# Kernel optimization log

Hardware: AMD Instinct MI355X
Metric: run time of the kernel (lower is better)

The kernel has to match this reference:

```python
import jax, jax.numpy as jnp
import numpy as np

EPS = 1e-5

def _layernorm(x, g, b):
    m = jnp.mean(x, axis=-1, keepdims=True)
    v = jnp.mean((x - m) ** 2, axis=-1, keepdims=True)
    return (x - m) * jax.lax.rsqrt(v + EPS) * g + b

def setup_inputs() -> dict:
    key = jax.random.key(0)
    ks = jax.random.split(key, 6)
    b, s, n = 1, 256, 512
    dim_msa, dim_pair, heads, dim_head = 64, 128, 8, 32
    dim_inner = heads * dim_head
    msa = jax.random.normal(ks[0], (b, s, n, dim_msa), dtype=jnp.float32)
    pairwise_repr = jax.random.normal(ks[1], (b, n, n, dim_pair), dtype=jnp.float32)
    mask = jnp.ones((b, n), dtype=bool)
    return {
        "msa": msa,
        "pairwise_repr": pairwise_repr,
        "ln_msa_g": jnp.ones((dim_msa,), jnp.float32),
        "ln_msa_b": jnp.zeros((dim_msa,), jnp.float32),
        "W_vg": jax.random.normal(ks[2], (dim_msa, dim_inner * 2), jnp.float32) * 0.02,
        "ln_pair_g": jnp.ones((dim_pair,), jnp.float32),
        "ln_pair_b": jnp.zeros((dim_pair,), jnp.float32),
        "W_pair": jax.random.normal(ks[3], (dim_pair, heads), jnp.float32) * 0.02,
        "W_out": jax.random.normal(ks[4], (dim_inner, dim_msa), jnp.float32) * 0.02,
        "mask": mask,
    }

def reference(msa, pairwise_repr, ln_msa_g, ln_msa_b, W_vg, ln_pair_g, ln_pair_b, W_pair, W_out, mask):
    heads, dim_head = 8, 32
    b, s, n, dim_msa = msa.shape
    # values and gates: LN -> LinearNoBias -> split (gv h d)
    vg = _layernorm(msa, ln_msa_g, ln_msa_b) @ W_vg            # [b,s,n,2*h*d]
    vg = vg.reshape(b, s, n, 2, heads, dim_head)
    vg = jnp.transpose(vg, (3, 0, 4, 1, 2, 5))                  # [2,b,h,s,n,d]
    values, gates = vg[0], jax.nn.sigmoid(vg[1])
    # pair bias: LN -> LinearNoBias -> [b,h,i,j]
    bias = _layernorm(pairwise_repr, ln_pair_g, ln_pair_b) @ W_pair  # [b,i,j,h]
    bias = jnp.transpose(bias, (0, 3, 1, 2))                    # [b,h,i,j]
    bias = jnp.where(mask[:, None, None, :], bias, -jnp.inf)
    weights = jax.nn.softmax(bias, axis=-1)                     # [b,h,i,j]
    out = jnp.einsum('bhij,bhsjd->bhsid', weights, values)      # [b,h,s,n,d]
    out = out * gates
    out = jnp.transpose(out, (0, 2, 3, 1, 4)).reshape(b, s, n, heads * dim_head)
    return out @ W_out                                          # [b,s,n,dim_msa]
```

## Files before the change

kernel.cpp:

```cpp
#include <hip/hip_runtime.h>
#include <hip/hip_bf16.h>


#define S 256
#define N 512
#define DM 64
#define DP 128
#define H 8
#define C 256
#define ROWS (S * N)

typedef __attribute__((ext_vector_type(8))) short bf16x8;
typedef __attribute__((ext_vector_type(4))) float f32x4;

static __device__ __forceinline__ float bf2f(unsigned int u16) {
    union { unsigned int i; float f; } x;
    x.i = u16 << 16;
    return x.f;
}
static __device__ __forceinline__ unsigned short f2bf(float f) {
    union { float f; unsigned int i; } x;
    x.f = f;
    unsigned int r = x.i + 0x7FFFu + ((x.i >> 16) & 1u);
    return (unsigned short)(r >> 16);
}
static __device__ __forceinline__ void gload16(const void* g, void* l) {
    __builtin_amdgcn_global_load_lds(
        (const __attribute__((address_space(1))) void*)g,
        (__attribute__((address_space(3))) void*)l, 16, 0, 0);
}

__global__ __launch_bounds__(256) void k0_prep(
    const float* __restrict__ Wvg, const float* __restrict__ g, const float* __restrict__ b,
    const float* __restrict__ Wout, const float* __restrict__ gp, const float* __restrict__ bp,
    const float* __restrict__ Wp,
    unsigned short* __restrict__ WTvg, float* __restrict__ biasvg, unsigned short* __restrict__ WoutT,
    float* __restrict__ Wg, float* __restrict__ sgcb)
{
    const int t = threadIdx.x;
    if (blockIdx.x < 2) {
        const int c = blockIdx.x * 256 + t;
        float bias = 0.f;
        unsigned short row[64];
#pragma unroll
        for (int k = 0; k < 64; k++) {
            const float w = Wvg[k * 512 + c];
            row[k] = f2bf(w * g[k]);
            bias = fmaf(w, b[k], bias);
        }
#pragma unroll
        for (int q = 0; q < 8; q++) *(uint4*)(WTvg + c * 64 + q * 8) = *(const uint4*)(row + q * 8);
        biasvg[c] = bias;
    } else if (blockIdx.x == 2) {
        const int m = t >> 2, c0 = (t & 3) * 64;
        unsigned short row[64];
#pragma unroll
        for (int q = 0; q < 64; q++) row[q] = f2bf(Wout[(c0 + q) * 64 + m]);
#pragma unroll
        for (int q = 0; q < 8; q++) *(uint4*)(WoutT + m * 256 + c0 + q * 8) = *(const uint4*)(row + q * 8);
    } else {
        if (t < 128) {
            const float gm = gp[t];
#pragma unroll
            for (int h = 0; h < 8; h++) Wg[t * 8 + h] = gm * Wp[t * 8 + h];
        } else if (t < 136) {
            const int h = t - 128;
            float sg = 0.f, cb = 0.f;
            for (int k = 0; k < 128; k++) {
                sg = fmaf(gp[k], Wp[k * 8 + h], sg);
                cb = fmaf(bp[k], Wp[k * 8 + h], cb);
            }
            sgcb[h] = sg;
            sgcb[8 + h] = cb;
        }
    }
}

__global__ __launch_bounds__(512, 4) void k1_vg_mfma(
    const float* __restrict__ msa, const unsigned short* __restrict__ WTvg,
    const float* __restrict__ biasvg,
    unsigned short* __restrict__ VT, unsigned short* __restrict__ G)
{
    __shared__ unsigned short wt[512 * 64];
    __shared__ unsigned short at[64 * 64];
    const int t = threadIdx.x, lane = t & 63, w = t >> 6;
    const int l15 = lane & 15, lgrp = lane >> 4;
    const int s = blockIdx.x >> 1;
    const int jbase = (blockIdx.x & 1) * 256;

#pragma unroll
    for (int q = 0; q < 8; q++) {
        const int u = q * 512 + t;
        const int c = u >> 3, ch = u & 7;
        const uint4 v = *(const uint4*)(WTvg + c * 64 + ch * 8);
        *(uint4*)((char*)wt + c * 128 + ((ch ^ (c & 7)) * 16)) = v;
    }
    float biasr[4];
    float bias2[4][4];
    if (w < 4) {
#pragma unroll
        for (int cf = 0; cf < 4; cf++) biasr[cf] = biasvg[w * 64 + cf * 16 + l15];
    } else {
#pragma unroll
        for (int cf = 0; cf < 4; cf++)
#pragma unroll
            for (int r = 0; r < 4; r++) bias2[cf][r] = biasvg[w * 64 + cf * 16 + lgrp * 4 + r];
    }

    for (int tile = 0; tile < 4; ++tile) {
        const int j0 = jbase + tile * 64;
        {
            const int r = t >> 3, kc = (t & 7) * 8;
            const float* src = msa + ((size_t)(s * 512 + j0 + r)) * 64 + kc;
            const float4 x0 = *(const float4*)src;
            const float4 x1 = *(const float4*)(src + 4);
            float s1 = x0.x + x0.y + x0.z + x0.w + x1.x + x1.y + x1.z + x1.w;
            float s2 = x0.x * x0.x + x0.y * x0.y + x0.z * x0.z + x0.w * x0.w
                     + x1.x * x1.x + x1.y * x1.y + x1.z * x1.z + x1.w * x1.w;
#pragma unroll
            for (int off = 1; off < 8; off <<= 1) {
                s1 += __shfl_xor(s1, off);
                s2 += __shfl_xor(s2, off);
            }
            const float m = s1 * (1.f / 64.f);
            const float inv = rsqrtf(s2 * (1.f / 64.f) - m * m + 1e-5f);
            unsigned short buf[8];
            buf[0] = f2bf((x0.x - m) * inv); buf[1] = f2bf((x0.y - m) * inv);
            buf[2] = f2bf((x0.z - m) * inv); buf[3] = f2bf((x0.w - m) * inv);
            buf[4] = f2bf((x1.x - m) * inv); buf[5] = f2bf((x1.y - m) * inv);
            buf[6] = f2bf((x1.z - m) * inv); buf[7] = f2bf((x1.w - m) * inv);
            *(uint4*)((char*)at + r * 128 + (((t & 7) ^ (r & 7)) * 16)) = *(const uint4*)buf;
        }
        __syncthreads();

        f32x4 acc[4][4];
#pragma unroll
        for (int rf = 0; rf < 4; rf++)
#pragma unroll
            for (int cf = 0; cf < 4; cf++) acc[rf][cf] = (f32x4){0.f, 0.f, 0.f, 0.f};

#pragma unroll
        for (int ks = 0; ks < 2; ks++) {
            bf16x8 bfr[4];
#pragma unroll
            for (int cf = 0; cf < 4; cf++) {
                const int c = w * 64 + cf * 16 + l15;
                bfr[cf] = *(const bf16x8*)((const char*)wt + c * 128 + (((ks * 4 + lgrp) ^ (c & 7)) * 16));
            }
#pragma unroll
            for (int rf = 0; rf < 4; rf++) {
                const int rr = rf * 16 + l15;
                const bf16x8 afr = *(const bf16x8*)((const char*)at + rr * 128 + (((ks * 4 + lgrp) ^ (rr & 7)) * 16));
                if (w < 4) {
#pragma unroll
                    for (int cf = 0; cf < 4; cf++)
                        acc[rf][cf] = __builtin_amdgcn_mfma_f32_16x16x32_bf16(afr, bfr[cf], acc[rf][cf], 0, 0, 0);
                } else {
#pragma unroll
                    for (int cf = 0; cf < 4; cf++)
                        acc[rf][cf] = __builtin_amdgcn_mfma_f32_16x16x32_bf16(bfr[cf], afr, acc[rf][cf], 0, 0, 0);
                }
            }
        }
        __syncthreads();

        if (w < 4) {
#pragma unroll
            for (int rf = 0; rf < 4; rf++)
#pragma unroll
                for (int cf = 0; cf < 4; cf++) {
                    const int c = w * 64 + cf * 16 + l15;
                    const int j = j0 + rf * 16 + lgrp * 4;
                    uint2 o;
                    o.x = (unsigned)f2bf(acc[rf][cf][0] + biasr[cf]) |
                          ((unsigned)f2bf(acc[rf][cf][1] + biasr[cf]) << 16);
                    o.y = (unsigned)f2bf(acc[rf][cf][2] + biasr[cf]) |
                          ((unsigned)f2bf(acc[rf][cf][3] + biasr[cf]) << 16);
                    *(uint2*)(VT + ((size_t)s * C + c) * N + j) = o;
                }
        } else {
#pragma unroll
            for (int rf = 0; rf < 4; rf++)
#pragma unroll
                for (int cf = 0; cf < 4; cf++) {
                    const int j = j0 + rf * 16 + l15;
                    const int cp = (w - 4) * 64 + cf * 16 + lgrp * 4;
                    float sg[4];
#pragma unroll
                    for (int r = 0; r < 4; r++)
                        sg[r] = 1.f / (1.f + __expf(-(acc[rf][cf][r] + bias2[cf][r])));
                    uint2 o;
                    o.x = (unsigned)f2bf(sg[0]) | ((unsigned)f2bf(sg[1]) << 16);
                    o.y = (unsigned)f2bf(sg[2]) | ((unsigned)f2bf(sg[3]) << 16);
                    *(uint2*)(G + ((size_t)(s * 512 + j)) * C + cp) = o;
                }
        }
    }
}

__global__ __launch_bounds__(512) void k2_bias_softmax(
    const float* __restrict__ pair, const float* __restrict__ Wg,
    const float* __restrict__ sgcb, unsigned short* __restrict__ Wt)
{
    __shared__ float bias_lds[H][N];
    const int i = blockIdx.x;
    const int t = threadIdx.x;
    const int sub = t & 15, rgrp = t >> 4;

    float wreg[2][4][8];
#pragma unroll
    for (int q = 0; q < 2; q++)
#pragma unroll
        for (int c = 0; c < 4; c++) {
            const int k = (q * 16 + sub) * 4 + c;
            const float4 w0 = *(const float4*)(Wg + k * 8);
            const float4 w1 = *(const float4*)(Wg + k * 8 + 4);
            wreg[q][c][0] = w0.x; wreg[q][c][1] = w0.y; wreg[q][c][2] = w0.z; wreg[q][c][3] = w0.w;
            wreg[q][c][4] = w1.x; wreg[q][c][5] = w1.y; wreg[q][c][6] = w1.z; wreg[q][c][7] = w1.w;
        }
    float sgr[8], cbr[8];
#pragma unroll
    for (int h = 0; h < 8; h++) { sgr[h] = sgcb[h]; cbr[h] = sgcb[8 + h]; }

    for (int pass = 0; pass < 16; ++pass) {
        const int r = pass * 32 + rgrp;
        const float* px = pair + ((size_t)i * N + r) * DP;
        const float4 x0 = *(const float4*)(px + (0 * 16 + sub) * 4);
        const float4 x1 = *(const float4*)(px + (1 * 16 + sub) * 4);
        float s1 = x0.x + x0.y + x0.z + x0.w + x1.x + x1.y + x1.z + x1.w;
        float s2 = x0.x * x0.x + x0.y * x0.y + x0.z * x0.z + x0.w * x0.w
                 + x1.x * x1.x + x1.y * x1.y + x1.z * x1.z + x1.w * x1.w;
#pragma unroll
        for (int off = 1; off < 16; off <<= 1) {
            s1 += __shfl_xor(s1, off);
            s2 += __shfl_xor(s2, off);
        }
        const float m = s1 * (1.f / 128.f);
        const float inv = rsqrtf(s2 * (1.f / 128.f) - m * m + 1e-5f);

        float dots[8];
#pragma unroll
        for (int h = 0; h < 8; h++) dots[h] = 0.f;
        const float xs[2][4] = {{x0.x, x0.y, x0.z, x0.w}, {x1.x, x1.y, x1.z, x1.w}};
#pragma unroll
        for (int q = 0; q < 2; q++)
#pragma unroll
            for (int c = 0; c < 4; c++)
#pragma unroll
                for (int h = 0; h < 8; h++) dots[h] = fmaf(xs[q][c], wreg[q][c][h], dots[h]);
#pragma unroll
        for (int off = 1; off < 16; off <<= 1)
#pragma unroll
            for (int h = 0; h < 8; h++) dots[h] += __shfl_xor(dots[h], off);

        if (sub == 0) {
#pragma unroll
            for (int h = 0; h < 8; h++)
                bias_lds[h][r] = inv * (dots[h] - m * sgr[h]) + cbr[h];
        }
    }
    __syncthreads();

    const int lane = t & 63, h = t >> 6;
    float v[8];
    float mx = -1e30f;
#pragma unroll
    for (int q = 0; q < 8; q++) {
        v[q] = bias_lds[h][q * 64 + lane];
        mx = fmaxf(mx, v[q]);
    }
#pragma unroll
    for (int off = 32; off > 0; off >>= 1) mx = fmaxf(mx, __shfl_xor(mx, off));
    float sum = 0.f;
#pragma unroll
    for (int q = 0; q < 8; q++) {
        v[q] = __expf(v[q] - mx);
        sum += v[q];
    }
#pragma unroll
    for (int off = 32; off > 0; off >>= 1) sum += __shfl_xor(sum, off);
    const float rs = 1.f / sum;
#pragma unroll
    for (int q = 0; q < 8; q++)
        Wt[((size_t)h * N + i) * N + q * 64 + lane] = f2bf(v[q] * rs);
}

__global__ __launch_bounds__(256, 2) void k3_fused_out(
    const unsigned short* __restrict__ Wt, const unsigned short* __restrict__ VT,
    const unsigned short* __restrict__ G, const unsigned short* __restrict__ WoutT,
    float* __restrict__ out)
{
    __shared__ unsigned short a_lds[64 * 64];
    __shared__ unsigned short b_lds[128 * 64];
    __shared__ unsigned short g_lds[2 * 128 * 32];
    const int raw = blockIdx.x;
    const int bid = (raw & 7) * 64 + (raw >> 3);
    const int sp = bid >> 2;
    const int it = bid & 3;
    const int s0 = sp * 2, i0 = it * 128;
    const int t = threadIdx.x, lane = t & 63, w = t >> 6;
    const int l15 = lane & 15, lgrp = lane >> 4;
    const int wn = w >> 1, wi = w & 1;

    const unsigned short* srcA[2];
    const unsigned short* srcB[4];
    int dstA[2], dstB[4];
#pragma unroll
    for (int q = 0; q < 2; ++q) {
        const int slot = q * 256 + t;
        const int row = slot >> 3, chp = slot & 7;
        const int ch = chp ^ (row & 7);
        srcA[q] = VT + ((size_t)((s0 + (row >> 5)) * 256 + (row & 31))) * 512 + ch * 8;
        dstA[q] = slot * 16;
    }
#pragma unroll
    for (int q = 0; q < 4; ++q) {
        const int slot = q * 256 + t;
        const int row = slot >> 3, chp = slot & 7;
        const int ch = chp ^ (row & 7);
        srcB[q] = Wt + ((size_t)(i0 + row)) * 512 + ch * 8;
        dstB[q] = slot * 16;
    }

    f32x4 oacc[2][2][4];
#pragma unroll
    for (int s = 0; s < 2; s++)
#pragma unroll
        for (int f = 0; f < 2; f++)
#pragma unroll
            for (int mf = 0; mf < 4; mf++) oacc[s][f][mf] = (f32x4){0.f, 0.f, 0.f, 0.f};

    for (int h = 0; h < 8; ++h) {
        uint2 gpre[2][4];
#pragma unroll
        for (int fn = 0; fn < 2; ++fn)
#pragma unroll
            for (int fi = 0; fi < 4; ++fi)
                gpre[fn][fi] = *(const uint2*)(G +
                    ((size_t)((s0 + wn) * 512 + i0 + wi * 64 + fi * 16 + l15)) * 256 +
                    h * 32 + fn * 16 + lgrp * 4);

        f32x4 acc[2][4];
#pragma unroll
        for (int fn = 0; fn < 2; fn++)
#pragma unroll
            for (int fi = 0; fi < 4; fi++) acc[fn][fi] = (f32x4){0.f, 0.f, 0.f, 0.f};

        const int offA = h * 16384;
        const int offB = h * 262144;
        for (int kt = 0; kt < 8; ++kt) {
            const int j0 = kt * 64;
#pragma unroll
            for (int q = 0; q < 2; ++q) gload16(srcA[q] + offA + j0, (char*)a_lds + dstA[q]);
#pragma unroll
            for (int q = 0; q < 4; ++q) gload16(srcB[q] + offB + j0, (char*)b_lds + dstB[q]);
            __syncthreads();
#pragma unroll
            for (int ks = 0; ks < 2; ++ks) {
                bf16x8 af[2], bf[4];
#pragma unroll
                for (int fn = 0; fn < 2; ++fn) {
                    const int ra = wn * 32 + fn * 16 + l15;
                    af[fn] = *(const bf16x8*)((const char*)a_lds + ra * 128 + (((ks * 4 + lgrp) ^ (ra & 7)) * 16));
                }
#pragma unroll
                for (int fi = 0; fi < 4; ++fi) {
                    const int rb = wi * 64 + fi * 16 + l15;
                    bf[fi] = *(const bf16x8*)((const char*)b_lds + rb * 128 + (((ks * 4 + lgrp) ^ (rb & 7)) * 16));
                }
#pragma unroll
                for (int fn = 0; fn < 2; ++fn)
#pragma unroll
                    for (int fi = 0; fi < 4; ++fi)
                        acc[fn][fi] = __builtin_amdgcn_mfma_f32_16x16x32_bf16(af[fn], bf[fi], acc[fn][fi], 0, 0, 0);
            }
            __syncthreads();
        }

#pragma unroll
        for (int fn = 0; fn < 2; ++fn) {
            const int d0 = fn * 16 + lgrp * 4;
#pragma unroll
            for (int fi = 0; fi < 4; ++fi) {
                const int i = wi * 64 + fi * 16 + l15;
                const uint2 uu = gpre[fn][fi];
                const float g0 = bf2f(uu.x & 0xFFFFu), g1 = bf2f(uu.x >> 16);
                const float g2 = bf2f(uu.y & 0xFFFFu), g3 = bf2f(uu.y >> 16);
                uint2 o;
                o.x = (unsigned)f2bf(acc[fn][fi][0] * g0) | ((unsigned)f2bf(acc[fn][fi][1] * g1) << 16);
                o.y = (unsigned)f2bf(acc[fn][fi][2] * g2) | ((unsigned)f2bf(acc[fn][fi][3] * g3) << 16);
                *(uint2*)((char*)g_lds + wn * 8192 + i * 64 + (((d0 >> 3) ^ (i & 3)) * 16) + (d0 & 7) * 2) = o;
            }
        }
        __syncthreads();

        bf16x8 bw[4];
#pragma unroll
        for (int mf = 0; mf < 4; ++mf)
            bw[mf] = *(const bf16x8*)(WoutT + (mf * 16 + l15) * 256 + h * 32 + lgrp * 8);
#pragma unroll
        for (int s = 0; s < 2; ++s) {
#pragma unroll
            for (int f = 0; f < 2; ++f) {
                const int ra = w * 32 + f * 16 + l15;
                const bf16x8 af = *(const bf16x8*)((const char*)g_lds + s * 8192 + ra * 64 + ((lgrp ^ (ra & 3)) * 16));
#pragma unroll
                for (int mf = 0; mf < 4; ++mf)
                    oacc[s][f][mf] = __builtin_amdgcn_mfma_f32_16x16x32_bf16(af, bw[mf], oacc[s][f][mf], 0, 0, 0);
            }
        }
        __syncthreads();
    }

#pragma unroll
    for (int s = 0; s < 2; ++s)
#pragma unroll
        for (int f = 0; f < 2; ++f)
#pragma unroll
            for (int mf = 0; mf < 4; ++mf)
#pragma unroll
                for (int r = 0; r < 4; ++r) {
                    const size_t row = (size_t)(s0 + s) * 512 + i0 + w * 32 + f * 16 + lgrp * 4 + r;
                    out[row * 64 + mf * 16 + l15] = oacc[s][f][mf][r];
                }
}

extern "C" void kernel_launch(void* const* d_in, const int* in_sizes, int n_in,
                              void* d_out, int out_size, void* d_ws, size_t ws_size,
                              hipStream_t stream) {
    (void)in_sizes; (void)n_in; (void)out_size; (void)ws_size;
    const float* msa       = (const float*)d_in[0];
    const float* pair      = (const float*)d_in[1];
    const float* ln_msa_g  = (const float*)d_in[2];
    const float* ln_msa_b  = (const float*)d_in[3];
    const float* W_vg      = (const float*)d_in[4];
    const float* ln_pair_g = (const float*)d_in[5];
    const float* ln_pair_b = (const float*)d_in[6];
    const float* W_pair    = (const float*)d_in[7];
    const float* W_out     = (const float*)d_in[8];
    float* out = (float*)d_out;

    char* ws = (char*)d_ws;
    size_t off = 0;
    unsigned short* VT    = (unsigned short*)(ws + off); off += (size_t)ROWS * C * 2;
    unsigned short* G     = (unsigned short*)(ws + off); off += (size_t)ROWS * C * 2;
    unsigned short* Wt    = (unsigned short*)(ws + off); off += (size_t)H * N * N * 2;
    unsigned short* WTvg  = (unsigned short*)(ws + off); off += 512 * 64 * 2;
    float*          biasvg = (float*)(ws + off); off += 512 * 4;
    unsigned short* WoutT = (unsigned short*)(ws + off); off += 64 * 256 * 2;
    float*          Wg    = (float*)(ws + off); off += 128 * 8 * 4;
    float*          sgcb  = (float*)(ws + off); off += 16 * 4;

    k0_prep<<<4, 256, 0, stream>>>(W_vg, ln_msa_g, ln_msa_b, W_out, ln_pair_g, ln_pair_b, W_pair,
                                   WTvg, biasvg, WoutT, Wg, sgcb);
    k2_bias_softmax<<<512, 512, 0, stream>>>(pair, Wg, sgcb, Wt);
    k1_vg_mfma<<<512, 512, 0, stream>>>(msa, WTvg, biasvg, VT, G);
    k3_fused_out<<<512, 256, 0, stream>>>(Wt, VT, G, WoutT, out);
}
```

Before: 203.5 us.

## Merge bias-softmax and value/gate projection kernels into one interleaved launch

Combines the pair-bias softmax kernel and the MSA value/gate MFMA kernel into a single 1024-block launch, with even blocks doing the softmax and odd blocks doing the projection. Independent memory-bound and compute-bound work can then run concurrently, and one launch gap disappears. The projection path now keeps its weight fragments in registers loaded straight from global memory instead of staging 64 KB in LDS, so shared memory drops to 16 KB, but register pressure rises.

```diff
diff --git a/kernel.cpp b/kernel.cpp
--- a/kernel.cpp
+++ b/kernel.cpp
@@ -76,213 +76,209 @@
     }
 }
 
-__global__ __launch_bounds__(512, 4) void k1_vg_mfma(
+__global__ __launch_bounds__(512) void k12_fused(
     const float* __restrict__ msa, const unsigned short* __restrict__ WTvg,
     const float* __restrict__ biasvg,
-    unsigned short* __restrict__ VT, unsigned short* __restrict__ G)
+    unsigned short* __restrict__ VT, unsigned short* __restrict__ G,
+    const float* __restrict__ pair, const float* __restrict__ Wg,
+    const float* __restrict__ sgcb, unsigned short* __restrict__ Wt)
 {
-    __shared__ unsigned short wt[512 * 64];
-    __shared__ unsigned short at[64 * 64];
-    const int t = threadIdx.x, lane = t & 63, w = t >> 6;
-    const int l15 = lane & 15, lgrp = lane >> 4;
-    const int s = blockIdx.x >> 1;
-    const int jbase = (blockIdx.x & 1) * 256;
-
-#pragma unroll
-    for (int q = 0; q < 8; q++) {
-        const int u = q * 512 + t;
-        const int c = u >> 3, ch = u & 7;
-        const uint4 v = *(const uint4*)(WTvg + c * 64 + ch * 8);
-        *(uint4*)((char*)wt + c * 128 + ((ch ^ (c & 7)) * 16)) = v;
-    }
-    float biasr[4];
-    float bias2[4][4];
-    if (w < 4) {
-#pragma unroll
-        for (int cf = 0; cf < 4; cf++) biasr[cf] = biasvg[w * 64 + cf * 16 + l15];
-    } else {
-#pragma unroll
-        for (int cf = 0; cf < 4; cf++)
-#pragma unroll
-            for (int r = 0; r < 4; r++) bias2[cf][r] = biasvg[w * 64 + cf * 16 + lgrp * 4 + r];
-    }
-
-    for (int tile = 0; tile < 4; ++tile) {
-        const int j0 = jbase + tile * 64;
-        {
-            const int r = t >> 3, kc = (t & 7) * 8;
-            const float* src = msa + ((size_t)(s * 512 + j0 + r)) * 64 + kc;
-            const float4 x0 = *(const float4*)src;
-            const float4 x1 = *(const float4*)(src + 4);
+    __shared__ __align__(16) char smem[16384];
+    const int t = threadIdx.x;
+
+    if ((blockIdx.x & 1) == 0) {
+        float (*bias_lds)[N] = (float(*)[N])smem;
+        const int i = blockIdx.x >> 1;
+        const int sub = t & 15, rgrp = t >> 4;
+
+        float wreg[2][4][8];
+#pragma unroll
+        for (int q = 0; q < 2; q++)
+#pragma unroll
+            for (int c = 0; c < 4; c++) {
+                const int k = (q * 16 + sub) * 4 + c;
+                const float4 w0 = *(const float4*)(Wg + k * 8);
+                const float4 w1 = *(const float4*)(Wg + k * 8 + 4);
+                wreg[q][c][0] = w0.x; wreg[q][c][1] = w0.y; wreg[q][c][2] = w0.z; wreg[q][c][3] = w0.w;
+                wreg[q][c][4] = w1.x; wreg[q][c][5] = w1.y; wreg[q][c][6] = w1.z; wreg[q][c][7] = w1.w;
+            }
+        float sgr[8], cbr[8];
+#pragma unroll
+        for (int h = 0; h < 8; h++) { sgr[h] = sgcb[h]; cbr[h] = sgcb[8 + h]; }
+
+        for (int pass = 0; pass < 16; ++pass) {
+            const int r = pass * 32 + rgrp;
+            const float* px = pair + ((size_t)i * N + r) * DP;
+            const float4 x0 = *(const float4*)(px + sub * 4);
+            const float4 x1 = *(const float4*)(px + 64 + sub * 4);
             float s1 = x0.x + x0.y + x0.z + x0.w + x1.x + x1.y + x1.z + x1.w;
             float s2 = x0.x * x0.x + x0.y * x0.y + x0.z * x0.z + x0.w * x0.w
                      + x1.x * x1.x + x1.y * x1.y + x1.z * x1.z + x1.w * x1.w;
 #pragma unroll
-            for (int off = 1; off < 8; off <<= 1) {
+            for (int off = 1; off < 16; off <<= 1) {
                 s1 += __shfl_xor(s1, off);
                 s2 += __shfl_xor(s2, off);
             }
-            const float m = s1 * (1.f / 64.f);
-            const float inv = rsqrtf(s2 * (1.f / 64.f) - m * m + 1e-5f);
-            unsigned short buf[8];
-            buf[0] = f2bf((x0.x - m) * inv); buf[1] = f2bf((x0.y - m) * inv);
-            buf[2] = f2bf((x0.z - m) * inv); buf[3] = f2bf((x0.w - m) * inv);
-            buf[4] = f2bf((x1.x - m) * inv); buf[5] = f2bf((x1.y - m) * inv);
-            buf[6] = f2bf((x1.z - m) * inv); buf[7] = f2bf((x1.w - m) * inv);
-            *(uint4*)((char*)at + r * 128 + (((t & 7) ^ (r & 7)) * 16)) = *(const uint4*)buf;
+            const float m = s1 * (1.f / 128.f);
+            const float inv = rsqrtf(s2 * (1.f / 128.f) - m * m + 1e-5f);
+
+            float dots[8];
+#pragma unroll
+            for (int h = 0; h < 8; h++) dots[h] = 0.f;
+            const float xs[2][4] = {{x0.x, x0.y, x0.z, x0.w}, {x1.x, x1.y, x1.z, x1.w}};
+#pragma unroll
+            for (int q = 0; q < 2; q++)
+#pragma unroll
+                for (int c = 0; c < 4; c++)
+#pragma unroll
+                    for (int h = 0; h < 8; h++) dots[h] = fmaf(xs[q][c], wreg[q][c][h], dots[h]);
+#pragma unroll
+            for (int off = 1; off < 16; off <<= 1)
+#pragma unroll
+                for (int h = 0; h < 8; h++) dots[h] += __shfl_xor(dots[h], off);
+
+            if (sub == 0) {
+#pragma unroll
+                for (int h = 0; h < 8; h++)
+                    bias_lds[h][r] = inv * (dots[h] - m * sgr[h]) + cbr[h];
+            }
         }
         __syncthreads();
 
-        f32x4 acc[4][4];
-#pragma unroll
-        for (int rf = 0; rf < 4; rf++)
-#pragma unroll
-            for (int cf = 0; cf < 4; cf++) acc[rf][cf] = (f32x4){0.f, 0.f, 0.f, 0.f};
-
-#pragma unroll
-        for (int ks = 0; ks < 2; ks++) {
-            bf16x8 bfr[4];
-#pragma unroll
-            for (int cf = 0; cf < 4; cf++) {
+        const int lane = t & 63, h = t >> 6;
+        float v[8];
+        float mx = -1e30f;
+#pragma unroll
+        for (int q = 0; q < 8; q++) {
+            v[q] = bias_lds[h][q * 64 + lane];
+            mx = fmaxf(mx, v[q]);
+        }
+#pragma unroll
+        for (int off = 32; off > 0; off >>= 1) mx = fmaxf(mx, __shfl_xor(mx, off));
+        float sum = 0.f;
+#pragma unroll
+        for (int q = 0; q < 8; q++) {
+            v[q] = __expf(v[q] - mx);
+            sum += v[q];
+        }
+#pragma unroll
+        for (int off = 32; off > 0; off >>= 1) sum += __shfl_xor(sum, off);
+        const float rs = 1.f / sum;
+#pragma unroll
+        for (int q = 0; q < 8; q++)
+            Wt[((size_t)h * N + i) * N + q * 64 + lane] = f2bf(v[q] * rs);
+    } else {
+        unsigned short* at = (unsigned short*)smem;
+        const int bid1 = blockIdx.x >> 1;
+        const int lane = t & 63, w = t >> 6;
+        const int l15 = lane & 15, lgrp = lane >> 4;
+        const int s = bid1 >> 1;
+        const int jbase = (bid1 & 1) * 256;
+
+        bf16x8 bfr[4][2];
+#pragma unroll
+        for (int cf = 0; cf < 4; cf++)
+#pragma unroll
+            for (int ks = 0; ks < 2; ks++) {
                 const int c = w * 64 + cf * 16 + l15;
-                bfr[cf] = *(const bf16x8*)((const char*)wt + c * 128 + (((ks * 4 + lgrp) ^ (c & 7)) * 16));
-            }
-#pragma unroll
-            for (int rf = 0; rf < 4; rf++) {
-                const int rr = rf * 16 + l15;
-                const bf16x8 afr = *(const bf16x8*)((const char*)at + rr * 128 + (((ks * 4 + lgrp) ^ (rr & 7)) * 16));
-                if (w < 4) {
-#pragma unroll
-                    for (int cf = 0; cf < 4; cf++)
-                        acc[rf][cf] = __builtin_amdgcn_mfma_f32_16x16x32_bf16(afr, bfr[cf], acc[rf][cf], 0, 0, 0);
-                } else {
-#pragma unroll
-                    for (int cf = 0; cf < 4; cf++)
-                        acc[rf][cf] = __builtin_amdgcn_mfma_f32_16x16x32_bf16(bfr[cf], afr, acc[rf][cf], 0, 0, 0);
+                bfr[cf][ks] = *(const bf16x8*)(WTvg + c * 64 + ks * 32 + lgrp * 8);
+            }
+        float biasr[4];
+        float bias2[4][4];
+        if (w < 4) {
+#pragma unroll
+            for (int cf = 0; cf < 4; cf++) biasr[cf] = biasvg[w * 64 + cf * 16 + l15];
+        } else {
+#pragma unroll
+            for (int cf = 0; cf < 4; cf++)
+#pragma unroll
+                for (int r = 0; r < 4; r++) bias2[cf][r] = biasvg[w * 64 + cf * 16 + lgrp * 4 + r];
+        }
+
+        for (int tile = 0; tile < 4; ++tile) {
+            const int j0 = jbase + tile * 64;
+            {
+                const int r = t >> 3, kc = (t & 7) * 8;
+                const float* src = msa + ((size_t)(s * 512 + j0 + r)) * 64 + kc;
+                const float4 x0 = *(const float4*)src;
+                const float4 x1 = *(const float4*)(src + 4);
+                float s1 = x0.x + x0.y + x0.z + x0.w + x1.x + x1.y + x1.z + x1.w;
+                float s2 = x0.x * x0.x + x0.y * x0.y + x0.z * x0.z + x0.w * x0.w
+                         + x1.x * x1.x + x1.y * x1.y + x1.z * x1.z + x1.w * x1.w;
+#pragma unroll
+                for (int off = 1; off < 8; off <<= 1) {
+                    s1 += __shfl_xor(s1, off);
+                    s2 += __shfl_xor(s2, off);
                 }
-            }
-        }
-        __syncthreads();
-
-        if (w < 4) {
+                const float m = s1 * (1.f / 64.f);
+                const float inv = rsqrtf(s2 * (1.f / 64.f) - m * m + 1e-5f);
+                unsigned short buf[8];
+                buf[0] = f2bf((x0.x - m) * inv); buf[1] = f2bf((x0.y - m) * inv);
+                buf[2] = f2bf((x0.z - m) * inv); buf[3] = f2bf((x0.w - m) * inv);
+                buf[4] = f2bf((x1.x - m) * inv); buf[5] = f2bf((x1.y - m) * inv);
+                buf[6] = f2bf((x1.z - m) * inv); buf[7] = f2bf((x1.w - m) * inv);
+                *(uint4*)((char*)at + r * 128 + (((t & 7) ^ (r & 7)) * 16)) = *(const uint4*)buf;
+            }
+            __syncthreads();
+
+            f32x4 acc[4][4];
 #pragma unroll
             for (int rf = 0; rf < 4; rf++)
 #pragma unroll
-                for (int cf = 0; cf < 4; cf++) {
-                    const int c = w * 64 + cf * 16 + l15;
-                    const int j = j0 + rf * 16 + lgrp * 4;
-                    uint2 o;
-                    o.x = (unsigned)f2bf(acc[rf][cf][0] + biasr[cf]) |
-                          ((unsigned)f2bf(acc[rf][cf][1] + biasr[cf]) << 16);
-                    o.y = (unsigned)f2bf(acc[rf][cf][2] + biasr[cf]) |
-                          ((unsigned)f2bf(acc[rf][cf][3] + biasr[cf]) << 16);
-                    *(uint2*)(VT + ((size_t)s * C + c) * N + j) = o;
+                for (int cf = 0; cf < 4; cf++) acc[rf][cf] = (f32x4){0.f, 0.f, 0.f, 0.f};
+
+#pragma unroll
+            for (int ks = 0; ks < 2; ks++) {
+#pragma unroll
+                for (int rf = 0; rf < 4; rf++) {
+                    const int rr = rf * 16 + l15;
+                    const bf16x8 afr = *(const bf16x8*)((const char*)at + rr * 128 + (((ks * 4 + lgrp) ^ (rr & 7)) * 16));
+                    if (w < 4) {
+#pragma unroll
+                        for (int cf = 0; cf < 4; cf++)
+                            acc[rf][cf] = __builtin_amdgcn_mfma_f32_16x16x32_bf16(afr, bfr[cf][ks], acc[rf][cf], 0, 0, 0);
+                    } else {
+#pragma unroll
+                        for (int cf = 0; cf < 4; cf++)
+                            acc[rf][cf] = __builtin_amdgcn_mfma_f32_16x16x32_bf16(bfr[cf][ks], afr, acc[rf][cf], 0, 0, 0);
+                    }
                 }
-        } else {
-#pragma unroll
-            for (int rf = 0; rf < 4; rf++)
-#pragma unroll
-                for (int cf = 0; cf < 4; cf++) {
-                    const int j = j0 + rf * 16 + l15;
-                    const int cp = (w - 4) * 64 + cf * 16 + lgrp * 4;
-                    float sg[4];
-#pragma unroll
-                    for (int r = 0; r < 4; r++)
-                        sg[r] = 1.f / (1.f + __expf(-(acc[rf][cf][r] + bias2[cf][r])));
-                    uint2 o;
-                    o.x = (unsigned)f2bf(sg[0]) | ((unsigned)f2bf(sg[1]) << 16);
-                    o.y = (unsigned)f2bf(sg[2]) | ((unsigned)f2bf(sg[3]) << 16);
-                    *(uint2*)(G + ((size_t)(s * 512 + j)) * C + cp) = o;
-                }
+            }
+            __syncthreads();
+
+            if (w < 4) {
+#pragma unroll
+                for (int rf = 0; rf < 4; rf++)
+#pragma unroll
+                    for (int cf = 0; cf < 4; cf++) {
+                        const int c = w * 64 + cf * 16 + l15;
+                        const int j = j0 + rf * 16 + lgrp * 4;
+                        uint2 o;
+                        o.x = (unsigned)f2bf(acc[rf][cf][0] + biasr[cf]) |
+                              ((unsigned)f2bf(acc[rf][cf][1] + biasr[cf]) << 16);
+                        o.y = (unsigned)f2bf(acc[rf][cf][2] + biasr[cf]) |
+                              ((unsigned)f2bf(acc[rf][cf][3] + biasr[cf]) << 16);
+                        *(uint2*)(VT + ((size_t)s * C + c) * N + j) = o;
+                    }
+            } else {
+#pragma unroll
+                for (int rf = 0; rf < 4; rf++)
+#pragma unroll
+                    for (int cf = 0; cf < 4; cf++) {
+                        const int j = j0 + rf * 16 + l15;
+                        const int cp = (w - 4) * 64 + cf * 16 + lgrp * 4;
+                        float sg[4];
+#pragma unroll
+                        for (int r = 0; r < 4; r++)
+                            sg[r] = 1.f / (1.f + __expf(-(acc[rf][cf][r] + bias2[cf][r])));
+                        uint2 o;
+                        o.x = (unsigned)f2bf(sg[0]) | ((unsigned)f2bf(sg[1]) << 16);
+                        o.y = (unsigned)f2bf(sg[2]) | ((unsigned)f2bf(sg[3]) << 16);
+                        *(uint2*)(G + ((size_t)(s * 512 + j)) * C + cp) = o;
+                    }
+            }
         }
     }
-}
-
-__global__ __launch_bounds__(512) void k2_bias_softmax(
-    const float* __restrict__ pair, const float* __restrict__ Wg,
-    const float* __restrict__ sgcb, unsigned short* __restrict__ Wt)
-{
-    __shared__ float bias_lds[H][N];
-    const int i = blockIdx.x;
-    const int t = threadIdx.x;
-    const int sub = t & 15, rgrp = t >> 4;
-
-    float wreg[2][4][8];
-#pragma unroll
-    for (int q = 0; q < 2; q++)
-#pragma unroll
-        for (int c = 0; c < 4; c++) {
-            const int k = (q * 16 + sub) * 4 + c;
-            const float4 w0 = *(const float4*)(Wg + k * 8);
-            const float4 w1 = *(const float4*)(Wg + k * 8 + 4);
-            wreg[q][c][0] = w0.x; wreg[q][c][1] = w0.y; wreg[q][c][2] = w0.z; wreg[q][c][3] = w0.w;
-            wreg[q][c][4] = w1.x; wreg[q][c][5] = w1.y; wreg[q][c][6] = w1.z; wreg[q][c][7] = w1.w;
-        }
-    float sgr[8], cbr[8];
-#pragma unroll
-    for (int h = 0; h < 8; h++) { sgr[h] = sgcb[h]; cbr[h] = sgcb[8 + h]; }
-
-    for (int pass = 0; pass < 16; ++pass) {
-        const int r = pass * 32 + rgrp;
-        const float* px = pair + ((size_t)i * N + r) * DP;
-        const float4 x0 = *(const float4*)(px + (0 * 16 + sub) * 4);
-        const float4 x1 = *(const float4*)(px + (1 * 16 + sub) * 4);
-        float s1 = x0.x + x0.y + x0.z + x0.w + x1.x + x1.y + x1.z + x1.w;
-        float s2 = x0.x * x0.x + x0.y * x0.y + x0.z * x0.z + x0.w * x0.w
-                 + x1.x * x1.x + x1.y * x1.y + x1.z * x1.z + x1.w * x1.w;
-#pragma unroll
-        for (int off = 1; off < 16; off <<= 1) {
-            s1 += __shfl_xor(s1, off);
-            s2 += __shfl_xor(s2, off);
-        }
-        const float m = s1 * (1.f / 128.f);
-        const float inv = rsqrtf(s2 * (1.f / 128.f) - m * m + 1e-5f);
-
-        float dots[8];
-#pragma unroll
-        for (int h = 0; h < 8; h++) dots[h] = 0.f;
-        const float xs[2][4] = {{x0.x, x0.y, x0.z, x0.w}, {x1.x, x1.y, x1.z, x1.w}};
-#pragma unroll
-        for (int q = 0; q < 2; q++)
-#pragma unroll
-            for (int c = 0; c < 4; c++)
-#pragma unroll
-                for (int h = 0; h < 8; h++) dots[h] = fmaf(xs[q][c], wreg[q][c][h], dots[h]);
-#pragma unroll
-        for (int off = 1; off < 16; off <<= 1)
-#pragma unroll
-            for (int h = 0; h < 8; h++) dots[h] += __shfl_xor(dots[h], off);
-
-        if (sub == 0) {
-#pragma unroll
-            for (int h = 0; h < 8; h++)
-                bias_lds[h][r] = inv * (dots[h] - m * sgr[h]) + cbr[h];
-        }
-    }
-    __syncthreads();
-
-    const int lane = t & 63, h = t >> 6;
-    float v[8];
-    float mx = -1e30f;
-#pragma unroll
-    for (int q = 0; q < 8; q++) {
-        v[q] = bias_lds[h][q * 64 + lane];
-        mx = fmaxf(mx, v[q]);
-    }
-#pragma unroll
-    for (int off = 32; off > 0; off >>= 1) mx = fmaxf(mx, __shfl_xor(mx, off));
-    float sum = 0.f;
-#pragma unroll
-    for (int q = 0; q < 8; q++) {
-        v[q] = __expf(v[q] - mx);
-        sum += v[q];
-    }
-#pragma unroll
-    for (int off = 32; off > 0; off >>= 1) sum += __shfl_xor(sum, off);
-    const float rs = 1.f / sum;
-#pragma unroll
-    for (int q = 0; q < 8; q++)
-        Wt[((size_t)h * N + i) * N + q * 64 + lane] = f2bf(v[q] * rs);
 }
 
 __global__ __launch_bounds__(256, 2) void k3_fused_out(
@@ -453,7 +449,6 @@
 
     k0_prep<<<4, 256, 0, stream>>>(W_vg, ln_msa_g, ln_msa_b, W_out, ln_pair_g, ln_pair_b, W_pair,
                                    WTvg, biasvg, WoutT, Wg, sgcb);
-    k2_bias_softmax<<<512, 512, 0, stream>>>(pair, Wg, sgcb, Wt);
-    k1_vg_mfma<<<512, 512, 0, stream>>>(msa, WTvg, biasvg, VT, G);
+    k12_fused<<<1024, 512, 0, stream>>>(msa, WTvg, biasvg, VT, G, pair, Wg, sgcb, Wt);
     k3_fused_out<<<512, 256, 0, stream>>>(Wt, VT, G, WoutT, out);
 }
```

New measurement: 204.8 us. Within noise of the previous version (+0.7%).
